# Kernel tuning notes

Measured on AMD Instinct MI355X. Metric: run time of the kernel, lower is better.

The kernel has to match this reference:

```python
import jax, jax.numpy as jnp
import numpy as np

N0, N1, N2 = 65536, 8192, 1024   # node counts per depth (pool factor 8, as in original m1*2=8)
DEG = 6                          # avg degree of k-space neighbor graphs
K = 10                           # number of Gaussian kernels in GMMConv


def _pool_graph(n_fine):
    # bidirectional edges between each group of 8 nodes and its representative (last node of group)
    mem = jnp.arange(n_fine)
    rep = (mem // 8) * 8 + 7
    return jnp.concatenate([mem, rep]), jnp.concatenate([rep, mem])


def setup_inputs() -> dict:
    key = jax.random.key(0)
    ks = list(jax.random.split(key, 40))
    E1, E2, E3 = DEG * N0, DEG * N1, DEG * N2
    d = {}
    d['n_feat'] = jax.random.normal(ks[0], (N0, 2), jnp.float32)
    d['src1'] = jax.random.randint(ks[1], (E1,), 0, N0)
    d['dst1'] = jax.random.randint(ks[2], (E1,), 0, N0)
    d['pkor1'] = 0.5 * jax.random.normal(ks[3], (E1, 2), jnp.float32)
    d['src2'] = jax.random.randint(ks[4], (E2,), 0, N1)
    d['dst2'] = jax.random.randint(ks[5], (E2,), 0, N1)
    d['pkor2'] = 0.5 * jax.random.normal(ks[6], (E2, 2), jnp.float32)
    d['src3'] = jax.random.randint(ks[7], (E3,), 0, N2)
    d['dst3'] = jax.random.randint(ks[8], (E3,), 0, N2)
    d['pkor3'] = 0.5 * jax.random.normal(ks[9], (E3, 2), jnp.float32)
    d['pm1_src'], d['pm1_dst'] = _pool_graph(N0)
    d['pm2_src'], d['pm2_dst'] = _pool_graph(N1)
    d['idx1'] = jnp.arange(N1) * 8 + 7
    d['idx2'] = jnp.arange(N2) * 8 + 7

    def lin(k, fi, fo):
        return jax.random.normal(k, (fi, K * fo), jnp.float32) / np.float32(np.sqrt(fi * K))

    d['W1'] = lin(ks[10], 2, 32)
    d['mu1'] = jax.random.normal(ks[11], (K, 2), jnp.float32)
    d['is1'] = jax.random.uniform(ks[12], (K, 2), jnp.float32, 0.5, 1.5)
    d['b1'] = 0.01 * jax.random.normal(ks[13], (32,), jnp.float32)
    d['W2'] = lin(ks[14], 32, 64)
    d['mu2'] = jax.random.normal(ks[15], (K, 2), jnp.float32)
    d['is2'] = jax.random.uniform(ks[16], (K, 2), jnp.float32, 0.5, 1.5)
    d['W3'] = lin(ks[17], 64, 128)
    d['mu3'] = jax.random.normal(ks[18], (K, 2), jnp.float32)
    d['is3'] = jax.random.uniform(ks[19], (K, 2), jnp.float32, 0.5, 1.5)
    d['W4'] = lin(ks[20], 192, 64)
    d['mu4'] = jax.random.normal(ks[21], (K, 2), jnp.float32)
    d['is4'] = jax.random.uniform(ks[22], (K, 2), jnp.float32, 0.5, 1.5)
    d['W5'] = lin(ks[23], 96, 40)
    d['mu5'] = jax.random.normal(ks[24], (K, 2), jnp.float32)
    d['is5'] = jax.random.uniform(ks[25], (K, 2), jnp.float32, 0.5, 1.5)
    d['b5'] = 0.01 * jax.random.normal(ks[26], (40,), jnp.float32)
    return d


def gmm_conv(x, W, mu, inv_sigma, src, dst, pseudo, n, bias=None):
    # DGL GMMConv, aggregator 'mean': h=fc(x) -> (N,K,F); gaussian edge weights over 2D pseudo coords
    h = (x @ W).reshape(x.shape[0], K, -1)                                   # (N,K,F)
    diff = pseudo[:, None, :] - mu[None, :, :]                               # (E,K,2)
    gw = jnp.exp(-0.5 * jnp.sum(diff * diff * (inv_sigma[None] ** 2), -1))   # (E,K)
    msg = h[src] * gw[:, :, None]                                            # (E,K,F)
    s = jax.ops.segment_sum(msg, dst, num_segments=n)
    deg = jax.ops.segment_sum(jnp.ones(dst.shape, x.dtype), dst, num_segments=n)
    out = jnp.sum(s / jnp.maximum(deg, 1.0)[:, None, None], axis=1)          # mean over edges, sum over kernels
    return out if bias is None else out + bias


def max_reduce(h, src, dst, n):
    # DGL update_all(copy_u, max): nodes with no in-edges get 0
    m = jax.ops.segment_max(h[src], dst, num_segments=n)
    deg = jax.ops.segment_sum(jnp.ones(dst.shape, h.dtype), dst, num_segments=n)
    return jnp.where(deg[:, None] > 0, m, jnp.zeros((), h.dtype))


def reference(n_feat, src1, dst1, pkor1, src2, dst2, pkor2, src3, dst3, pkor3,
              pm1_src, pm1_dst, pm2_src, pm2_dst, idx1, idx2,
              W1, mu1, is1, b1, W2, mu2, is2, W3, mu3, is3,
              W4, mu4, is4, W5, mu5, is5, b5):
    # encoder
    out0 = jax.nn.relu(gmm_conv(n_feat, W1, mu1, is1, src1, dst1, pkor1, N0, b1))      # (N0,32) skip0
    h = max_reduce(out0, pm1_src, pm1_dst, N0)[idx1]                                    # MaxPool -> (N1,32)
    out1 = jax.nn.relu(gmm_conv(h, W2, mu2, is2, src2, dst2, pkor2, N1))                # (N1,64) skip1
    h = max_reduce(out1, pm2_src, pm2_dst, N1)[idx2]                                    # MaxPool -> (N2,64)
    out2 = jax.nn.relu(gmm_conv(h, W3, mu3, is3, src3, dst3, pkor3, N2))                # (N2,128) bottleneck
    # decoder
    hu = jnp.zeros((N1, out2.shape[1]), out2.dtype).at[idx2].set(out2)
    hu = max_reduce(hu, pm2_src, pm2_dst, N1)                                           # UpSample -> (N1,128)
    out3 = jax.nn.relu(gmm_conv(jnp.concatenate([hu, out1], 1), W4, mu4, is4,
                                src2, dst2, pkor2, N1))                                 # (N1,64)
    hu = jnp.zeros((N0, out3.shape[1]), out3.dtype).at[idx1].set(out3)
    hu = max_reduce(hu, pm1_src, pm1_dst, N0)                                           # UpSample -> (N0,64)
    return jnp.tanh(gmm_conv(jnp.concatenate([hu, out0], 1), W5, mu5, is5,
                             src1, dst1, pkor1, N0, b5))                                # (N0,40)
```

## Files before the change

### kernel.cpp

```cpp
#include <hip/hip_runtime.h>


#define N0C 65536
#define N1C 8192
#define N2C 1024
#define KK 10

typedef _Float16 half2t __attribute__((ext_vector_type(2)));
typedef _Float16 half4 __attribute__((ext_vector_type(4)));
typedef _Float16 f16x8 __attribute__((ext_vector_type(8)));
typedef float f32x4 __attribute__((ext_vector_type(4)));

static inline int cdiv(long long a, long long b) { return (int)((a + b - 1) / b); }

__device__ __forceinline__ size_t fragi(int r, int kd, int KDT) {
    return ((size_t)(r >> 4) * KDT + (kd >> 5)) * 64 + ((kd >> 3) & 3) * 16 + (r & 15);
}


__global__ __launch_bounds__(256)
void k_hist3(const int* __restrict__ d1, const int* __restrict__ d2,
             const int* __restrict__ d3, int* __restrict__ g1,
             int* __restrict__ g2, int* __restrict__ g3,
             int E1, int E2, int E3) {
    int i = blockIdx.x * 256 + threadIdx.x;
    if (i < E1) atomicAdd(&g1[d1[i]], 1);
    else if (i < E1 + E2) atomicAdd(&g2[d2[i - E1]], 1);
    else if (i < E1 + E2 + E3) atomicAdd(&g3[d3[i - E1 - E2]], 1);
}

__device__ __forceinline__ void map_graph(int b, int& lb, int& gi) {
    if (b < 256) { gi = 0; lb = b; }
    else if (b < 288) { gi = 1; lb = b - 256; }
    else { gi = 2; lb = b - 288; }
}

__global__ __launch_bounds__(256)
void k_scanall(const int* __restrict__ deg1, int* __restrict__ off1, float* __restrict__ inv1,
               const int* __restrict__ deg2, int* __restrict__ off2, float* __restrict__ inv2,
               const int* __restrict__ deg3, int* __restrict__ off3, float* __restrict__ inv3,
               int E1, int E2, int E3) {
    __shared__ int s[256];
    int lb, gi; map_graph(blockIdx.x, lb, gi);
    const int* deg = gi == 0 ? deg1 : (gi == 1 ? deg2 : deg3);
    int* off = gi == 0 ? off1 : (gi == 1 ? off2 : off3);
    float* inv = gi == 0 ? inv1 : (gi == 1 ? inv2 : inv3);
    int n = gi == 0 ? N0C : (gi == 1 ? N1C : N2C);
    int E = gi == 0 ? E1 : (gi == 1 ? E2 : E3);
    int pre = 0;
    for (int i = threadIdx.x; i < lb * 256; i += 256) pre += deg[i];
    s[threadIdx.x] = pre;
    __syncthreads();
#pragma unroll
    for (int d = 128; d > 0; d >>= 1) {
        if (threadIdx.x < d) s[threadIdx.x] += s[threadIdx.x + d];
        __syncthreads();
    }
    int base = s[0];
    __syncthreads();
    int i = lb * 256 + threadIdx.x;
    int v = deg[i];
    s[threadIdx.x] = v;
    __syncthreads();
#pragma unroll
    for (int d = 1; d < 256; d <<= 1) {
        int t = (threadIdx.x >= d) ? s[threadIdx.x - d] : 0;
        __syncthreads();
        s[threadIdx.x] += t;
        __syncthreads();
    }
    off[i] = base + s[threadIdx.x] - v;
    inv[i] = 1.0f / fmaxf((float)v, 1.0f);
    if (i == n - 1) off[n] = E;
}

__global__ __launch_bounds__(256)
void k_scatter3(const int* __restrict__ s1, const int* __restrict__ d1,
                const float* __restrict__ p1, const int* __restrict__ o1,
                int* __restrict__ c1, int* __restrict__ cs1, float2* __restrict__ cp1,
                const int* __restrict__ s2, const int* __restrict__ d2,
                const float* __restrict__ p2, const int* __restrict__ o2,
                int* __restrict__ c2, int* __restrict__ cs2, float2* __restrict__ cp2,
                const int* __restrict__ s3, const int* __restrict__ d3,
                const float* __restrict__ p3, const int* __restrict__ o3,
                int* __restrict__ c3, int* __restrict__ cs3, float2* __restrict__ cp3,
                int E1, int E2, int E3) {
    int i = blockIdx.x * 256 + threadIdx.x;
    const int* src; const int* dst; const float* pk; const int* off;
    int* cur; int* csrc; float2* cpk; int e;
    if (i < E1) { src = s1; dst = d1; pk = p1; off = o1; cur = c1; csrc = cs1; cpk = cp1; e = i; }
    else if (i < E1 + E2) { src = s2; dst = d2; pk = p2; off = o2; cur = c2; csrc = cs2; cpk = cp2; e = i - E1; }
    else if (i < E1 + E2 + E3) { src = s3; dst = d3; pk = p3; off = o3; cur = c3; csrc = cs3; cpk = cp3; e = i - E1 - E2; }
    else return;
    int d = dst[e];
    int p = off[d] + atomicAdd(&cur[d], 1);
    csrc[p] = src[e];
    cpk[p] = reinterpret_cast<const float2*>(pk)[e];
}

__global__ __launch_bounds__(256)
void k_gw(const float2* __restrict__ cp1, const float2* __restrict__ cp2,
          const float2* __restrict__ cp3,
          const float* __restrict__ mu1, const float* __restrict__ is1,
          const float* __restrict__ mu5, const float* __restrict__ is5,
          const float* __restrict__ mu2, const float* __restrict__ is2,
          const float* __restrict__ mu4, const float* __restrict__ is4,
          const float* __restrict__ mu3, const float* __restrict__ is3,
          float* __restrict__ g1, float* __restrict__ g5, float* __restrict__ g2,
          float* __restrict__ g4, float* __restrict__ g3,
          int E1, int E2, int E3) {
    int i = blockIdx.x * 256 + threadIdx.x;
    const float2* cp; const float* mu; const float* isg; float* g; int e;
    if (i < E1) { cp = cp1; mu = mu1; isg = is1; g = g1; e = i; }
    else if (i < 2 * E1) { cp = cp1; mu = mu5; isg = is5; g = g5; e = i - E1; }
    else if (i < 2 * E1 + E2) { cp = cp2; mu = mu2; isg = is2; g = g2; e = i - 2 * E1; }
    else if (i < 2 * E1 + 2 * E2) { cp = cp2; mu = mu4; isg = is4; g = g4; e = i - 2 * E1 - E2; }
    else if (i < 2 * E1 + 2 * E2 + E3) { cp = cp3; mu = mu3; isg = is3; g = g3; e = i - 2 * E1 - 2 * E2; }
    else return;
    float2 pk = cp[e];
    float o[KK];
#pragma unroll
    for (int k = 0; k < KK; ++k) {
        float dx = (pk.x - mu[2 * k]) * isg[2 * k];
        float dy = (pk.y - mu[2 * k + 1]) * isg[2 * k + 1];
        o[k] = __expf(-0.5f * (dx * dx + dy * dy));
    }
    float4* gp = reinterpret_cast<float4*>(g + (size_t)e * 12);
    gp[0] = make_float4(o[0], o[1], o[2], o[3]);
    gp[1] = make_float4(o[4], o[5], o[6], o[7]);
    gp[2] = make_float4(o[8], o[9], 0.f, 0.f);
}

#define LOAD_G(gw, j, G)                                                     \
    float G[KK];                                                             \
    {                                                                        \
        const float4* gp_ = reinterpret_cast<const float4*>((gw) + (size_t)(j) * 12); \
        float4 g0_ = gp_[0], g1_ = gp_[1]; float2 g2_ = *reinterpret_cast<const float2*>(gp_ + 2); \
        G[0] = g0_.x; G[1] = g0_.y; G[2] = g0_.z; G[3] = g0_.w;              \
        G[4] = g1_.x; G[5] = g1_.y; G[6] = g1_.z; G[7] = g1_.w;              \
        G[8] = g2_.x; G[9] = g2_.y;                                          \
    }

#define LOAD_G2(gwp, j, G)                                                   \
    {                                                                        \
        const float4* gp_ = reinterpret_cast<const float4*>((gwp) + (size_t)(j) * 12); \
        float4 g0_ = gp_[0], g1_ = gp_[1];                                   \
        float2 g2_ = *reinterpret_cast<const float2*>(gp_ + 2);              \
        G[0] = g0_.x; G[1] = g0_.y; G[2] = g0_.z; G[3] = g0_.w;              \
        G[4] = g1_.x; G[5] = g1_.y; G[6] = g1_.z; G[7] = g1_.w;              \
        G[8] = g2_.x; G[9] = g2_.y;                                          \
    }

__global__ __launch_bounds__(256)
void k_prep_wt(const float* __restrict__ W1, const float* __restrict__ W2,
               const float* __restrict__ W3, const float* __restrict__ W4,
               const float* __restrict__ W5,
               _Float16* __restrict__ T2,
               _Float16* __restrict__ T3, _Float16* __restrict__ T4,
               _Float16* __restrict__ T5, int* __restrict__ degs, int degn) {
    int id = blockIdx.x * 256 + threadIdx.x;
    if (id < degn) degs[id] = 0;
    if (id < 20480) {
        int f = id / 320, kc = id % 320;
        T2[fragi(f, kc, 10) * 8 + (kc & 7)] = (_Float16)W2[(kc % 32) * 640 + (kc / 32) * 64 + f];
        return;
    }
    id -= 20480;
    if (id < 81920) {
        int f = id / 640, kc = id % 640;
        T3[fragi(f, kc, 20) * 8 + (kc & 7)] = (_Float16)W3[(kc % 64) * 1280 + (kc / 64) * 128 + f];
        return;
    }
    id -= 81920;
    if (id < 122880) {
        int f = id / 1920, kc = id % 1920;
        T4[fragi(f, kc, 60) * 8 + (kc & 7)] = (_Float16)W4[(kc % 192) * 640 + (kc / 192) * 64 + f];
        return;
    }
    id -= 122880;
    if (id < 46080) {
        int f = id / 960, kc = id % 960;
        float v = (f < 40) ? W5[(kc % 96) * 400 + (kc / 96) * 40 + f] : 0.0f;
        T5[fragi(f, kc, 30) * 8 + (kc & 7)] = (_Float16)v;
    }
}

__global__ __launch_bounds__(256, 3)
void k_l1(const float* __restrict__ x, const int* __restrict__ off,
          const int* __restrict__ csrc, const float* __restrict__ gw,
          const float* __restrict__ inv, const float* __restrict__ W1,
          const float* __restrict__ b1, _Float16* __restrict__ out0,
          _Float16* __restrict__ hp1) {
    __shared__ float Ws[640];
    __shared__ float bs[32];
    for (int i = threadIdx.x; i < 640; i += 256) Ws[i] = W1[i];
    if (threadIdx.x < 32) bs[threadIdx.x] = b1[threadIdx.x];
    __syncthreads();
    int n = blockIdx.x * 256 + threadIdx.x;
    float a0[KK], a1[KK];
#pragma unroll
    for (int k = 0; k < KK; ++k) { a0[k] = 0.f; a1[k] = 0.f; }
    int j0 = off[n], j1 = off[n + 1];
    int j = j0;
    for (; j + 1 < j1; j += 2) {
        int sa = csrc[j];
        int sb = csrc[j + 1];
        LOAD_G(gw, j, Ga)
        LOAD_G(gw, j + 1, Gb)
        float2 xa = reinterpret_cast<const float2*>(x)[sa];
        float2 xb = reinterpret_cast<const float2*>(x)[sb];
#pragma unroll
        for (int k = 0; k < KK; ++k) {
            a0[k] = fmaf(Ga[k], xa.x, a0[k]);
            a1[k] = fmaf(Ga[k], xa.y, a1[k]);
            a0[k] = fmaf(Gb[k], xb.x, a0[k]);
            a1[k] = fmaf(Gb[k], xb.y, a1[k]);
        }
    }
    if (j < j1) {
        int sa = csrc[j];
        LOAD_G(gw, j, Ga)
        float2 xa = reinterpret_cast<const float2*>(x)[sa];
#pragma unroll
        for (int k = 0; k < KK; ++k) {
            a0[k] = fmaf(Ga[k], xa.x, a0[k]);
            a1[k] = fmaf(Ga[k], xa.y, a1[k]);
        }
    }
    float iv = inv[n];
#pragma unroll
    for (int k = 0; k < KK; ++k) { a0[k] *= iv; a1[k] *= iv; }
    _Float16* orow = out0 + (size_t)n * 32;
    _Float16* prow = hp1 + (size_t)(n >> 3) * 32;
#pragma unroll
    for (int f4 = 0; f4 < 8; ++f4) {
        float v0 = bs[f4 * 4], v1 = bs[f4 * 4 + 1], v2 = bs[f4 * 4 + 2], v3 = bs[f4 * 4 + 3];
#pragma unroll
        for (int k = 0; k < KK; ++k) {
            const float* w0 = Ws + k * 32 + f4 * 4;
            const float* w1 = w0 + 320;
            v0 += a0[k] * w0[0] + a1[k] * w1[0];
            v1 += a0[k] * w0[1] + a1[k] * w1[1];
            v2 += a0[k] * w0[2] + a1[k] * w1[2];
            v3 += a0[k] * w0[3] + a1[k] * w1[3];
        }
        v0 = fmaxf(v0, 0.f); v1 = fmaxf(v1, 0.f);
        v2 = fmaxf(v2, 0.f); v3 = fmaxf(v3, 0.f);
        half4 o;
        o[0] = (_Float16)v0; o[1] = (_Float16)v1;
        o[2] = (_Float16)v2; o[3] = (_Float16)v3;
        *reinterpret_cast<half4*>(orow + f4 * 4) = o;
#pragma unroll
        for (int d = 1; d < 8; d <<= 1) {
            v0 = fmaxf(v0, __shfl_xor(v0, d));
            v1 = fmaxf(v1, __shfl_xor(v1, d));
            v2 = fmaxf(v2, __shfl_xor(v2, d));
            v3 = fmaxf(v3, __shfl_xor(v3, d));
        }
        if ((threadIdx.x & 7) == 0) {
            half4 p;
            p[0] = (_Float16)v0; p[1] = (_Float16)v1;
            p[2] = (_Float16)v2; p[3] = (_Float16)v3;
            *reinterpret_cast<half4*>(prow + f4 * 4) = p;
        }
    }
}

template <int TPN>
__global__ __launch_bounds__(256, 3)
void k_aggx(const _Float16* __restrict__ xp, const int* __restrict__ off,
            const int* __restrict__ csrc, const float* __restrict__ gw,
            const float* __restrict__ inv, _Float16* __restrict__ agg, int N) {
    constexpr int CIN = TPN * 4;
    constexpr int KDT = KK * CIN / 32;
    int tid = threadIdx.x;
    int nl = tid / TPN, tt = tid - nl * TPN;
    int node = blockIdx.x * (256 / TPN) + nl;
    if (node >= N) return;
    float a[KK][4];
#pragma unroll
    for (int k = 0; k < KK; ++k)
#pragma unroll
        for (int e = 0; e < 4; ++e) a[k][e] = 0.f;
    int j0 = off[node], j1 = off[node + 1];
    int j = j0;
    for (; j + 1 < j1; j += 2) {
        int sa = csrc[j];
        int sb = csrc[j + 1];
        LOAD_G(gw, j, Ga)
        LOAD_G(gw, j + 1, Gb)
        half4 ha = *reinterpret_cast<const half4*>(xp + (size_t)sa * CIN + 4 * tt);
        half4 hb = *reinterpret_cast<const half4*>(xp + (size_t)sb * CIN + 4 * tt);
        float a0 = ha[0], a1 = ha[1], a2 = ha[2], a3 = ha[3];
        float b0 = hb[0], b1 = hb[1], b2 = hb[2], b3 = hb[3];
#pragma unroll
        for (int k = 0; k < KK; ++k) {
            a[k][0] = fmaf(Ga[k], a0, a[k][0]);
            a[k][1] = fmaf(Ga[k], a1, a[k][1]);
            a[k][2] = fmaf(Ga[k], a2, a[k][2]);
            a[k][3] = fmaf(Ga[k], a3, a[k][3]);
            a[k][0] = fmaf(Gb[k], b0, a[k][0]);
            a[k][1] = fmaf(Gb[k], b1, a[k][1]);
            a[k][2] = fmaf(Gb[k], b2, a[k][2]);
            a[k][3] = fmaf(Gb[k], b3, a[k][3]);
        }
    }
    if (j < j1) {
        int sa = csrc[j];
        LOAD_G(gw, j, Ga)
        half4 ha = *reinterpret_cast<const half4*>(xp + (size_t)sa * CIN + 4 * tt);
        float a0 = ha[0], a1 = ha[1], a2 = ha[2], a3 = ha[3];
#pragma unroll
        for (int k = 0; k < KK; ++k) {
            a[k][0] = fmaf(Ga[k], a0, a[k][0]);
            a[k][1] = fmaf(Ga[k], a1, a[k][1]);
            a[k][2] = fmaf(Ga[k], a2, a[k][2]);
            a[k][3] = fmaf(Ga[k], a3, a[k][3]);
        }
    }
    float iv = inv[node];
#pragma unroll
    for (int k = 0; k < KK; ++k) {
        half4 o;
        o[0] = (_Float16)(a[k][0] * iv); o[1] = (_Float16)(a[k][1] * iv);
        o[2] = (_Float16)(a[k][2] * iv); o[3] = (_Float16)(a[k][3] * iv);
        int kd = k * CIN + 4 * tt;
        *reinterpret_cast<half4*>(agg + fragi(node, kd, KDT) * 8 + (kd & 7)) = o;
    }
}

template <int CA, int CB, int WPB, int NPW, int NT, int ACT, int FST, int OUTH>
__global__ __launch_bounds__(WPB * 64)
void k_aggf4(const _Float16* __restrict__ xA, const _Float16* __restrict__ xB,
             const int* __restrict__ off, const int* __restrict__ csrc,
             const float* __restrict__ gw, const float* __restrict__ inv,
             const _Float16* __restrict__ Wt, const float* __restrict__ bias,
             void* __restrict__ outv, int nodeBase) {
    constexpr int CIN = CA + CB;
    constexpr int PAIRS = CIN / 2;
    constexpr int P = (PAIRS + 63) / 64;
    constexpr int KDT = KK * CIN / 32;
    constexpr int STRIDE = KK * CIN + 8;
    __shared__ _Float16 lds[16 * STRIDE];
    const int lane = threadIdx.x & 63;
    const int wv = threadIdx.x >> 6;
    int j0u[NPW], degu[NPW], sallu[NPW];
#pragma unroll
    for (int u = 0; u < NPW; ++u) {
        const int node = __builtin_amdgcn_readfirstlane(nodeBase + blockIdx.x * 16 + wv * NPW + u);
        j0u[u] = __builtin_amdgcn_readfirstlane(off[node]);
        int j1 = __builtin_amdgcn_readfirstlane(off[node + 1]);
        degu[u] = j1 - j0u[u];
        int pl = (degu[u] > 0) ? (j0u[u] + (lane < degu[u] ? lane : degu[u] - 1)) : 0;
        sallu[u] = csrc[pl];
    }
#pragma unroll
    for (int u = 0; u < NPW; ++u) {
        const int nl = wv * NPW + u;
        const int node = __builtin_amdgcn_readfirstlane(nodeBase + blockIdx.x * 16 + nl);
        const int j0 = j0u[u];
        const int deg = degu[u];
        const int sall = sallu[u];
        float a[KK][2 * P];
#pragma unroll
        for (int k = 0; k < KK; ++k)
#pragma unroll
            for (int p = 0; p < 2 * P; ++p) a[k][p] = 0.f;
        int e = 0;
        for (; e + 1 < deg; e += 2) {
            int sa = __builtin_amdgcn_readlane(sall, e);
            int sb = __builtin_amdgcn_readlane(sall, e + 1);
            int gj = __builtin_amdgcn_readfirstlane(j0 + e);
            float Ga[KK], Gb[KK];
            LOAD_G2(gw, gj, Ga)
            LOAD_G2(gw, gj + 1, Gb)
            float xa0[P], xa1[P], xb0[P], xb1[P];
#pragma unroll
            for (int p = 0; p < P; ++p) {
                int c0 = 2 * (lane + 64 * p);
                xa0[p] = 0.f; xa1[p] = 0.f; xb0[p] = 0.f; xb1[p] = 0.f;
                if (c0 < CIN) {
                    bool useA = c0 < CA;
                    const _Float16* qa = useA ? (xA + (size_t)(sa >> 3) * CA + c0)
                                              : (xB + (size_t)sa * CB + (c0 - CA));
                    const _Float16* qb = useA ? (xA + (size_t)(sb >> 3) * CA + c0)
                                              : (xB + (size_t)sb * CB + (c0 - CA));
                    half2t ha = *reinterpret_cast<const half2t*>(qa);
                    half2t hb = *reinterpret_cast<const half2t*>(qb);
                    xa0[p] = ha[0]; xa1[p] = ha[1];
                    xb0[p] = hb[0]; xb1[p] = hb[1];
                }
            }
#pragma unroll
            for (int k = 0; k < KK; ++k)
#pragma unroll
                for (int p = 0; p < P; ++p) {
                    a[k][2 * p] = fmaf(Ga[k], xa0[p], a[k][2 * p]);
                    a[k][2 * p + 1] = fmaf(Ga[k], xa1[p], a[k][2 * p + 1]);
                    a[k][2 * p] = fmaf(Gb[k], xb0[p], a[k][2 * p]);
                    a[k][2 * p + 1] = fmaf(Gb[k], xb1[p], a[k][2 * p + 1]);
                }
        }
        if (e < deg) {
            int sa = __builtin_amdgcn_readlane(sall, e);
            int gj = __builtin_amdgcn_readfirstlane(j0 + e);
            float Ga[KK];
            LOAD_G2(gw, gj, Ga)
            float xa0[P], xa1[P];
#pragma unroll
            for (int p = 0; p < P; ++p) {
                int c0 = 2 * (lane + 64 * p);
                xa0[p] = 0.f; xa1[p] = 0.f;
                if (c0 < CIN) {
                    const _Float16* qa = (c0 < CA) ? (xA + (size_t)(sa >> 3) * CA + c0)
                                                   : (xB + (size_t)sa * CB + (c0 - CA));
                    half2t ha = *reinterpret_cast<const half2t*>(qa);
                    xa0[p] = ha[0]; xa1[p] = ha[1];
                }
            }
#pragma unroll
            for (int k = 0; k < KK; ++k)
#pragma unroll
                for (int p = 0; p < P; ++p) {
                    a[k][2 * p] = fmaf(Ga[k], xa0[p], a[k][2 * p]);
                    a[k][2 * p + 1] = fmaf(Ga[k], xa1[p], a[k][2 * p + 1]);
                }
        }
        float iv = inv[node];
#pragma unroll
        for (int k = 0; k < KK; ++k)
#pragma unroll
            for (int p = 0; p < P; ++p) {
                int c0 = 2 * (lane + 64 * p);
                if (c0 < CIN) {
                    half2t o;
                    o[0] = (_Float16)(a[k][2 * p] * iv);
                    o[1] = (_Float16)(a[k][2 * p + 1] * iv);
                    *reinterpret_cast<half2t*>(&lds[nl * STRIDE + k * CIN + c0]) = o;
                }
            }
    }
    constexpr int PF = (KDT < 8) ? KDT : 8;
    const int lm = lane & 15;
    const int q = lane >> 4;
    const f16x8* bp = (const f16x8*)Wt + (size_t)wv * KDT * 64 + lane;
    f16x8 bfr[PF];
    if (wv < NT) {
#pragma unroll
        for (int i = 0; i < PF; ++i) bfr[i] = bp[(size_t)i * 64];
    }
    __syncthreads();
    if (wv < NT) {
        f32x4 acc = (f32x4){0.f, 0.f, 0.f, 0.f};
        f16x8 af = *reinterpret_cast<const f16x8*>(&lds[lm * STRIDE + q * 8]);
#pragma unroll
        for (int i = 0; i < KDT; ++i) {
            f16x8 afn;
            if (i + 1 < KDT)
                afn = *reinterpret_cast<const f16x8*>(&lds[lm * STRIDE + (i + 1) * 32 + q * 8]);
            f16x8 b = bfr[i % PF];
            if (i + PF < KDT) bfr[i % PF] = bp[(size_t)(i + PF) * 64];
            acc = __builtin_amdgcn_mfma_f32_16x16x32_f16(af, b, acc, 0, 0, 0);
            af = afn;
        }
        int f = wv * 16 + lm;
        if (f < FST) {
            float b = bias ? bias[f] : 0.0f;
#pragma unroll
            for (int r = 0; r < 4; ++r) {
                size_t node = (size_t)nodeBase + (size_t)blockIdx.x * 16 + q * 4 + r;
                float v = acc[r] + b;
                v = (ACT == 1) ? tanhf(v) : fmaxf(v, 0.0f);
                if (OUTH) ((_Float16*)outv)[node * FST + f] = (_Float16)v;
                else ((float*)outv)[node * FST + f] = v;
            }
        }
    }
}

template <int WB, int NT, int ITERS, int ACT, int FST, int OUTH, int POOL>
__global__ __launch_bounds__(WB * 64)
void k_gemm2(const _Float16* __restrict__ A, const _Float16* __restrict__ B,
             const float* __restrict__ bias, void* __restrict__ outv,
             _Float16* __restrict__ poolout, int M) {
    constexpr int KDT = ITERS;
    const int lane = threadIdx.x & 63;
    const int wv = threadIdx.x >> 6;
    const int lm = lane & 15;
    const int q = lane >> 4;
    const size_t m0 = (size_t)blockIdx.y * (WB * 16) + wv * 16;
    const size_t mblk = m0 >> 4;
    f32x4 acc[NT];
#pragma unroll
    for (int t = 0; t < NT; ++t) acc[t] = (f32x4){0.f, 0.f, 0.f, 0.f};
    const f16x8* ap = (const f16x8*)A + mblk * KDT * 64 + lane;
    const f16x8* bp = (const f16x8*)B + lane;
    f16x8 af = ap[0];
    f16x8 bf[NT];
#pragma unroll
    for (int t = 0; t < NT; ++t) bf[t] = bp[(size_t)t * KDT * 64];
#pragma unroll
    for (int i = 0; i < ITERS; ++i) {
        f16x8 afn; f16x8 bfn[NT];
        if (i + 1 < ITERS) {
            afn = ap[(size_t)(i + 1) * 64];
#pragma unroll
            for (int t = 0; t < NT; ++t)
                bfn[t] = bp[((size_t)t * KDT + i + 1) * 64];
        }
#pragma unroll
        for (int t = 0; t < NT; ++t)
            acc[t] = __builtin_amdgcn_mfma_f32_16x16x32_f16(af, bf[t], acc[t], 0, 0, 0);
        af = afn;
#pragma unroll
        for (int t = 0; t < NT; ++t) bf[t] = bfn[t];
    }
#pragma unroll
    for (int t = 0; t < NT; ++t) {
        int f = t * 16 + lm;
        if (f < FST) {
            float b = bias ? bias[f] : 0.0f;
            float vr[4];
#pragma unroll
            for (int r = 0; r < 4; ++r) {
                float v = acc[t][r] + b;
                vr[r] = (ACT == 1) ? tanhf(v) : fmaxf(v, 0.0f);
            }
#pragma unroll
            for (int r = 0; r < 4; ++r) {
                if (OUTH) ((_Float16*)outv)[(m0 + q * 4 + r) * (size_t)FST + f] = (_Float16)vr[r];
                else ((float*)outv)[(m0 + q * 4 + r) * (size_t)FST + f] = vr[r];
            }
            if (POOL) {
                float m = fmaxf(fmaxf(vr[0], vr[1]), fmaxf(vr[2], vr[3]));
                m = fmaxf(m, __shfl_xor(m, 16));
                if ((q & 1) == 0)
                    poolout[(size_t)((m0 >> 3) + (q >> 1)) * FST + f] = (_Float16)m;
            }
        }
    }
}

extern "C" void kernel_launch(void* const* d_in, const int* in_sizes, int n_in,
                              void* d_out, int out_size, void* d_ws, size_t ws_size,
                              hipStream_t stream) {
    const float* n_feat = (const float*)d_in[0];
    const int* src1 = (const int*)d_in[1];
    const int* dst1 = (const int*)d_in[2];
    const float* pkor1 = (const float*)d_in[3];
    const int* src2 = (const int*)d_in[4];
    const int* dst2 = (const int*)d_in[5];
    const float* pkor2 = (const float*)d_in[6];
    const int* src3 = (const int*)d_in[7];
    const int* dst3 = (const int*)d_in[8];
    const float* pkor3 = (const float*)d_in[9];
    const float* W1 = (const float*)d_in[16];
    const float* mu1 = (const float*)d_in[17];
    const float* is1 = (const float*)d_in[18];
    const float* b1 = (const float*)d_in[19];
    const float* W2 = (const float*)d_in[20];
    const float* mu2 = (const float*)d_in[21];
    const float* is2 = (const float*)d_in[22];
    const float* W3 = (const float*)d_in[23];
    const float* mu3 = (const float*)d_in[24];
    const float* is3 = (const float*)d_in[25];
    const float* W4 = (const float*)d_in[26];
    const float* mu4 = (const float*)d_in[27];
    const float* is4 = (const float*)d_in[28];
    const float* W5 = (const float*)d_in[29];
    const float* mu5 = (const float*)d_in[30];
    const float* is5 = (const float*)d_in[31];
    const float* b5 = (const float*)d_in[32];

    const int E1 = in_sizes[1], E2 = in_sizes[4], E3 = in_sizes[7];
    const int NT_ = N0C + N1C + N2C;

    char* w = (char*)d_ws;
    auto alloc = [&](size_t bytes) {
        void* p = (void*)w;
        w += (bytes + 255) & ~(size_t)255;
        return p;
    };
    int* degs = (int*)alloc((size_t)NT_ * 2 * 4);
    int* deg1 = degs, *deg2 = degs + N0C, *deg3 = degs + N0C + N1C;
    int* cur1 = degs + NT_, *cur2 = cur1 + N0C, *cur3 = cur2 + N1C;
    int* off1 = (int*)alloc(((size_t)N0C + 1) * 4);
    int* off2 = (int*)alloc(((size_t)N1C + 1) * 4);
    int* off3 = (int*)alloc(((size_t)N2C + 1) * 4);
    int* csrc1 = (int*)alloc((size_t)E1 * 4);
    float2* cpk1 = (float2*)alloc((size_t)E1 * 8);
    int* csrc2 = (int*)alloc((size_t)E2 * 4);
    float2* cpk2 = (float2*)alloc((size_t)E2 * 8);
    int* csrc3 = (int*)alloc((size_t)E3 * 4);
    float2* cpk3 = (float2*)alloc((size_t)E3 * 8);
    float* inv1 = (float*)alloc((size_t)N0C * 4);
    float* inv2 = (float*)alloc((size_t)N1C * 4);
    float* inv3 = (float*)alloc((size_t)N2C * 4);
    float* g1 = (float*)alloc(((size_t)2 * E1 + 2 * E2 + E3) * 12 * 4);
    float* g5 = g1 + (size_t)E1 * 12;
    float* g2 = g5 + (size_t)E1 * 12;
    float* g4 = g2 + (size_t)E2 * 12;
    float* g3 = g4 + (size_t)E2 * 12;
    _Float16* out0 = (_Float16*)alloc((size_t)N0C * 32 * 2);
    _Float16* out1 = (_Float16*)alloc((size_t)N1C * 64 * 2);
    _Float16* out2 = (_Float16*)alloc((size_t)N2C * 128 * 2);
    _Float16* out3 = (_Float16*)alloc((size_t)N1C * 64 * 2);
    _Float16* hp1 = (_Float16*)alloc((size_t)N1C * 32 * 2);
    _Float16* hp2 = (_Float16*)alloc((size_t)N2C * 64 * 2);
    _Float16* agg2 = (_Float16*)alloc((size_t)N1C * 320 * 2);
    _Float16* agg3 = (_Float16*)alloc((size_t)N2C * 640 * 2);
    _Float16* Wt2 = (_Float16*)alloc((size_t)64 * 320 * 2);
    _Float16* Wt3 = (_Float16*)alloc((size_t)128 * 640 * 2);
    _Float16* Wt4 = (_Float16*)alloc((size_t)64 * 1920 * 2);
    _Float16* Wt5 = (_Float16*)alloc((size_t)48 * 960 * 2);

    const int ET = E1 + E2 + E3;
    const int GT = 2 * E1 + 2 * E2 + E3;

    k_prep_wt<<<cdiv(271360, 256), 256, 0, stream>>>(W1, W2, W3, W4, W5,
                                                     Wt2, Wt3, Wt4, Wt5,
                                                     degs, NT_ * 2);
    k_hist3<<<cdiv(ET, 256), 256, 0, stream>>>(dst1, dst2, dst3, deg1, deg2, deg3, E1, E2, E3);
    k_scanall<<<292, 256, 0, stream>>>(deg1, off1, inv1, deg2, off2, inv2,
                                       deg3, off3, inv3, E1, E2, E3);
    k_scatter3<<<cdiv(ET, 256), 256, 0, stream>>>(
        src1, dst1, pkor1, off1, cur1, csrc1, cpk1,
        src2, dst2, pkor2, off2, cur2, csrc2, cpk2,
        src3, dst3, pkor3, off3, cur3, csrc3, cpk3, E1, E2, E3);
    k_gw<<<cdiv(GT, 256), 256, 0, stream>>>(
        cpk1, cpk2, cpk3, mu1, is1, mu5, is5, mu2, is2, mu4, is4, mu3, is3,
        g1, g5, g2, g4, g3, E1, E2, E3);

    k_l1<<<N0C / 256, 256, 0, stream>>>(n_feat, off1, csrc1, g1, inv1, W1, b1, out0, hp1);

    k_aggx<8><<<cdiv(N1C, 32), 256, 0, stream>>>(hp1, off2, csrc2, g2, inv2, agg2, N1C);
    k_gemm2<2, 4, 10, 0, 64, 1, 1><<<dim3(1, N1C / 32), 128, 0, stream>>>(agg2, Wt2, nullptr, out1, hp2, N1C);

    k_aggx<16><<<cdiv(N2C, 16), 256, 0, stream>>>(hp2, off3, csrc3, g3, inv3, agg3, N2C);
    k_gemm2<1, 8, 20, 0, 128, 1, 0><<<dim3(1, N2C / 16), 64, 0, stream>>>(agg3, Wt3, nullptr, out2, nullptr, N2C);

    k_aggf4<128, 64, 16, 1, 4, 0, 64, 1><<<N1C / 16, 1024, 0, stream>>>(
        out2, out1, off2, csrc2, g4, inv2, Wt4, nullptr, out3, 0);

    k_aggf4<64, 32, 8, 2, 3, 1, 40, 0><<<N0C / 16, 512, 0, stream>>>(
        out3, out0, off1, csrc1, g5, inv1, Wt5, b5, d_out, 0);
}
```

Baseline: 334.1 us.

## Split edge loops across threads and software-pipeline gather loads in aggregation kernels

k_l1 now uses two threads per node, each walking alternate edges, and combines their partial sums with a shuffle. The two threads split the output features, and the max-pool shuffle is remapped to match. k_aggx gains an ES parameter so several thread groups split one node's edges and reduce with xor-shuffles, with more blocks launched to match. k_aggf4 gains a PIPE mode, enabled for the last layer, that prefetches the next edge pair's Gaussian weights and features before doing the current FMAs. The goal is more parallelism and better hiding of latency on the irregular gathers, at the cost of extra shuffles, more registers and idle lanes when nodes have few edges.

Result: slower. 382.8 us (+14.6%).

```diff
diff --git a/kernel.cpp b/kernel.cpp
--- a/kernel.cpp
+++ b/kernel.cpp
@@ -131,16 +131,6 @@
     gp[2] = make_float4(o[8], o[9], 0.f, 0.f);
 }
 
-#define LOAD_G(gw, j, G)                                                     \
-    float G[KK];                                                             \
-    {                                                                        \
-        const float4* gp_ = reinterpret_cast<const float4*>((gw) + (size_t)(j) * 12); \
-        float4 g0_ = gp_[0], g1_ = gp_[1]; float2 g2_ = *reinterpret_cast<const float2*>(gp_ + 2); \
-        G[0] = g0_.x; G[1] = g0_.y; G[2] = g0_.z; G[3] = g0_.w;              \
-        G[4] = g1_.x; G[5] = g1_.y; G[6] = g1_.z; G[7] = g1_.w;              \
-        G[8] = g2_.x; G[9] = g2_.y;                                          \
-    }
-
 #define LOAD_G2(gwp, j, G)                                                   \
     {                                                                        \
         const float4* gp_ = reinterpret_cast<const float4*>((gwp) + (size_t)(j) * 12); \
@@ -196,44 +186,53 @@
     for (int i = threadIdx.x; i < 640; i += 256) Ws[i] = W1[i];
     if (threadIdx.x < 32) bs[threadIdx.x] = b1[threadIdx.x];
     __syncthreads();
-    int n = blockIdx.x * 256 + threadIdx.x;
+    int tid2 = blockIdx.x * 256 + threadIdx.x;
+    int n = tid2 >> 1;
+    int h = tid2 & 1;
     float a0[KK], a1[KK];
 #pragma unroll
     for (int k = 0; k < KK; ++k) { a0[k] = 0.f; a1[k] = 0.f; }
     int j0 = off[n], j1 = off[n + 1];
-    int j = j0;
-    for (; j + 1 < j1; j += 2) {
-        int sa = csrc[j];
-        int sb = csrc[j + 1];
-        LOAD_G(gw, j, Ga)
-        LOAD_G(gw, j + 1, Gb)
-        float2 xa = reinterpret_cast<const float2*>(x)[sa];
-        float2 xb = reinterpret_cast<const float2*>(x)[sb];
+    int j = j0 + h;
+    bool have = j < j1;
+    float Gc[KK]; float2 xc;
+    if (have) {
+        int s = csrc[j];
+        LOAD_G2(gw, j, Gc)
+        xc = reinterpret_cast<const float2*>(x)[s];
+    }
+    while (have) {
+        int jn = j + 2;
+        bool hn = jn < j1;
+        float Gn[KK]; float2 xn;
+        if (hn) {
+            int s = csrc[jn];
+            LOAD_G2(gw, jn, Gn)
+            xn = reinterpret_cast<const float2*>(x)[s];
+        }
 #pragma unroll
         for (int k = 0; k < KK; ++k) {
-            a0[k] = fmaf(Ga[k], xa.x, a0[k]);
-            a1[k] = fmaf(Ga[k], xa.y, a1[k]);
-            a0[k] = fmaf(Gb[k], xb.x, a0[k]);
-            a1[k] = fmaf(Gb[k], xb.y, a1[k]);
-        }
-    }
-    if (j < j1) {
-        int sa = csrc[j];
-        LOAD_G(gw, j, Ga)
-        float2 xa = reinterpret_cast<const float2*>(x)[sa];
-#pragma unroll
-        for (int k = 0; k < KK; ++k) {
-            a0[k] = fmaf(Ga[k], xa.x, a0[k]);
-            a1[k] = fmaf(Ga[k], xa.y, a1[k]);
+            a0[k] = fmaf(Gc[k], xc.x, a0[k]);
+            a1[k] = fmaf(Gc[k], xc.y, a1[k]);
+        }
+        j = jn; have = hn;
+        if (hn) {
+#pragma unroll
+            for (int k = 0; k < KK; ++k) Gc[k] = Gn[k];
+            xc = xn;
         }
     }
     float iv = inv[n];
 #pragma unroll
-    for (int k = 0; k < KK; ++k) { a0[k] *= iv; a1[k] *= iv; }
+    for (int k = 0; k < KK; ++k) {
+        a0[k] = (a0[k] + __shfl_xor(a0[k], 1)) * iv;
+        a1[k] = (a1[k] + __shfl_xor(a1[k], 1)) * iv;
+    }
     _Float16* orow = out0 + (size_t)n * 32;
-    _Float16* prow = hp1 + (size_t)(n >> 3) * 32;
-#pragma unroll
-    for (int f4 = 0; f4 < 8; ++f4) {
+    _Float16* prow = hp1 + (size_t)(tid2 >> 4) * 32;
+#pragma unroll
+    for (int t = 0; t < 4; ++t) {
+        int f4 = h * 4 + t;
         float v0 = bs[f4 * 4], v1 = bs[f4 * 4 + 1], v2 = bs[f4 * 4 + 2], v3 = bs[f4 * 4 + 3];
 #pragma unroll
         for (int k = 0; k < KK; ++k) {
@@ -251,13 +250,13 @@
         o[2] = (_Float16)v2; o[3] = (_Float16)v3;
         *reinterpret_cast<half4*>(orow + f4 * 4) = o;
 #pragma unroll
-        for (int d = 1; d < 8; d <<= 1) {
+        for (int d = 2; d < 16; d <<= 1) {
             v0 = fmaxf(v0, __shfl_xor(v0, d));
             v1 = fmaxf(v1, __shfl_xor(v1, d));
             v2 = fmaxf(v2, __shfl_xor(v2, d));
             v3 = fmaxf(v3, __shfl_xor(v3, d));
         }
-        if ((threadIdx.x & 7) == 0) {
+        if ((threadIdx.x & 15) == h) {
             half4 p;
             p[0] = (_Float16)v0; p[1] = (_Float16)v1;
             p[2] = (_Float16)v2; p[3] = (_Float16)v3;
@@ -266,16 +265,18 @@
     }
 }
 
-template <int TPN>
+template <int TPN, int ES>
 __global__ __launch_bounds__(256, 3)
 void k_aggx(const _Float16* __restrict__ xp, const int* __restrict__ off,
             const int* __restrict__ csrc, const float* __restrict__ gw,
             const float* __restrict__ inv, _Float16* __restrict__ agg, int N) {
     constexpr int CIN = TPN * 4;
     constexpr int KDT = KK * CIN / 32;
-    int tid = threadIdx.x;
-    int nl = tid / TPN, tt = tid - nl * TPN;
-    int node = blockIdx.x * (256 / TPN) + nl;
+    constexpr int TG = TPN * ES;
+    int gtid = blockIdx.x * 256 + threadIdx.x;
+    int node = gtid / TG;
+    int rem = threadIdx.x % TG;
+    int tt = rem % TPN, es = rem / TPN;
     if (node >= N) return;
     float a[KK][4];
 #pragma unroll
@@ -283,53 +284,62 @@
 #pragma unroll
         for (int e = 0; e < 4; ++e) a[k][e] = 0.f;
     int j0 = off[node], j1 = off[node + 1];
-    int j = j0;
-    for (; j + 1 < j1; j += 2) {
-        int sa = csrc[j];
-        int sb = csrc[j + 1];
-        LOAD_G(gw, j, Ga)
-        LOAD_G(gw, j + 1, Gb)
-        half4 ha = *reinterpret_cast<const half4*>(xp + (size_t)sa * CIN + 4 * tt);
-        half4 hb = *reinterpret_cast<const half4*>(xp + (size_t)sb * CIN + 4 * tt);
-        float a0 = ha[0], a1 = ha[1], a2 = ha[2], a3 = ha[3];
-        float b0 = hb[0], b1 = hb[1], b2 = hb[2], b3 = hb[3];
+    const _Float16* xb = xp + 4 * tt;
+    int j = j0 + es;
+    bool have = j < j1;
+    float Gc[KK]; half4 hc;
+    if (have) {
+        int s = csrc[j];
+        LOAD_G2(gw, j, Gc)
+        hc = *reinterpret_cast<const half4*>(xb + (size_t)s * CIN);
+    }
+    while (have) {
+        int jn = j + ES;
+        bool hn = jn < j1;
+        float Gn[KK]; half4 hx;
+        if (hn) {
+            int s = csrc[jn];
+            LOAD_G2(gw, jn, Gn)
+            hx = *reinterpret_cast<const half4*>(xb + (size_t)s * CIN);
+        }
+        float f0 = hc[0], f1 = hc[1], f2 = hc[2], f3 = hc[3];
 #pragma unroll
         for (int k = 0; k < KK; ++k) {
-            a[k][0] = fmaf(Ga[k], a0, a[k][0]);
-            a[k][1] = fmaf(Ga[k], a1, a[k][1]);
-            a[k][2] = fmaf(Ga[k], a2, a[k][2]);
-            a[k][3] = fmaf(Ga[k], a3, a[k][3]);
-            a[k][0] = fmaf(Gb[k], b0, a[k][0]);
-            a[k][1] = fmaf(Gb[k], b1, a[k][1]);
-            a[k][2] = fmaf(Gb[k], b2, a[k][2]);
-            a[k][3] = fmaf(Gb[k], b3, a[k][3]);
-        }
-    }
-    if (j < j1) {
-        int sa = csrc[j];
-        LOAD_G(gw, j, Ga)
-        half4 ha = *reinterpret_cast<const half4*>(xp + (size_t)sa * CIN + 4 * tt);
-        float a0 = ha[0], a1 = ha[1], a2 = ha[2], a3 = ha[3];
+            a[k][0] = fmaf(Gc[k], f0, a[k][0]);
+            a[k][1] = fmaf(Gc[k], f1, a[k][1]);
+            a[k][2] = fmaf(Gc[k], f2, a[k][2]);
+            a[k][3] = fmaf(Gc[k], f3, a[k][3]);
+        }
+        j = jn; have = hn;
+        if (hn) {
+#pragma unroll
+            for (int k = 0; k < KK; ++k) Gc[k] = Gn[k];
+            hc = hx;
+        }
+    }
+#pragma unroll
+    for (int d = TPN; d < TG; d <<= 1)
 #pragma unroll
         for (int k = 0; k < KK; ++k) {
-            a[k][0] = fmaf(Ga[k], a0, a[k][0]);
-            a[k][1] = fmaf(Ga[k], a1, a[k][1]);
-            a[k][2] = fmaf(Ga[k], a2, a[k][2]);
-            a[k][3] = fmaf(Ga[k], a3, a[k][3]);
-        }
-    }
-    float iv = inv[node];
-#pragma unroll
-    for (int k = 0; k < KK; ++k) {
-        half4 o;
-        o[0] = (_Float16)(a[k][0] * iv); o[1] = (_Float16)(a[k][1] * iv);
-        o[2] = (_Float16)(a[k][2] * iv); o[3] = (_Float16)(a[k][3] * iv);
-        int kd = k * CIN + 4 * tt;
-        *reinterpret_cast<half4*>(agg + fragi(node, kd, KDT) * 8 + (kd & 7)) = o;
-    }
-}
-
-template <int CA, int CB, int WPB, int NPW, int NT, int ACT, int FST, int OUTH>
+            a[k][0] += __shfl_xor(a[k][0], d);
+            a[k][1] += __shfl_xor(a[k][1], d);
+            a[k][2] += __shfl_xor(a[k][2], d);
+            a[k][3] += __shfl_xor(a[k][3], d);
+        }
+    if (es == 0) {
+        float iv = inv[node];
+#pragma unroll
+        for (int k = 0; k < KK; ++k) {
+            half4 o;
+            o[0] = (_Float16)(a[k][0] * iv); o[1] = (_Float16)(a[k][1] * iv);
+            o[2] = (_Float16)(a[k][2] * iv); o[3] = (_Float16)(a[k][3] * iv);
+            int kd = k * CIN + 4 * tt;
+            *reinterpret_cast<half4*>(agg + fragi(node, kd, KDT) * 8 + (kd & 7)) = o;
+        }
+    }
+}
+
+template <int CA, int CB, int WPB, int NPW, int NT, int ACT, int FST, int OUTH, int PIPE>
 __global__ __launch_bounds__(WPB * 64)
 void k_aggf4(const _Float16* __restrict__ xA, const _Float16* __restrict__ xB,
              const int* __restrict__ off, const int* __restrict__ csrc,
@@ -354,6 +364,51 @@
         int pl = (degu[u] > 0) ? (j0u[u] + (lane < degu[u] ? lane : degu[u] - 1)) : 0;
         sallu[u] = csrc[pl];
     }
+
+#define AGG_LOADP(I, GA, GB, XA0, XA1, XB0, XB1)                              \
+    {                                                                         \
+        int e0_ = 2 * (I);                                                    \
+        bool odd_ = (e0_ + 1) >= deg;                                         \
+        int e1c_ = odd_ ? deg - 1 : e0_ + 1;                                  \
+        int sa_ = __builtin_amdgcn_readlane(sall, e0_);                       \
+        int sb_ = __builtin_amdgcn_readlane(sall, e1c_);                      \
+        int gja_ = __builtin_amdgcn_readfirstlane(j0 + e0_);                  \
+        int gjb_ = __builtin_amdgcn_readfirstlane(j0 + e1c_);                 \
+        LOAD_G2(gw, gja_, GA)                                                 \
+        LOAD_G2(gw, gjb_, GB)                                                 \
+        if (odd_) {                                                           \
+            _Pragma("unroll")                                                 \
+            for (int k_ = 0; k_ < KK; ++k_) GB[k_] = 0.f;                     \
+        }                                                                     \
+        _Pragma("unroll")                                                     \
+        for (int p_ = 0; p_ < P; ++p_) {                                      \
+            int c0_ = 2 * (lane + 64 * p_);                                   \
+            XA0[p_] = 0.f; XA1[p_] = 0.f; XB0[p_] = 0.f; XB1[p_] = 0.f;       \
+            if (c0_ < CIN) {                                                  \
+                bool useA_ = c0_ < CA;                                        \
+                const _Float16* qa_ = useA_ ? (xA + (size_t)(sa_ >> 3) * CA + c0_) \
+                                            : (xB + (size_t)sa_ * CB + (c0_ - CA)); \
+                const _Float16* qb_ = useA_ ? (xA + (size_t)(sb_ >> 3) * CA + c0_) \
+                                            : (xB + (size_t)sb_ * CB + (c0_ - CA)); \
+                half2t ha_ = *reinterpret_cast<const half2t*>(qa_);           \
+                half2t hb_ = *reinterpret_cast<const half2t*>(qb_);           \
+                XA0[p_] = ha_[0]; XA1[p_] = ha_[1];                           \
+                XB0[p_] = hb_[0]; XB1[p_] = hb_[1];                           \
+            }                                                                 \
+        }                                                                     \
+    }
+
+#define AGG_FMA(GA, GB, XA0, XA1, XB0, XB1)                                   \
+    _Pragma("unroll")                                                         \
+    for (int k_ = 0; k_ < KK; ++k_)                                           \
+        _Pragma("unroll")                                                     \
+        for (int p_ = 0; p_ < P; ++p_) {                                      \
+            a[k_][2 * p_] = fmaf(GA[k_], XA0[p_], a[k_][2 * p_]);             \
+            a[k_][2 * p_ + 1] = fmaf(GA[k_], XA1[p_], a[k_][2 * p_ + 1]);     \
+            a[k_][2 * p_] = fmaf(GB[k_], XB0[p_], a[k_][2 * p_]);             \
+            a[k_][2 * p_ + 1] = fmaf(GB[k_], XB1[p_], a[k_][2 * p_ + 1]);     \
+        }
+
 #pragma unroll
     for (int u = 0; u < NPW; ++u) {
         const int nl = wv * NPW + u;
@@ -366,65 +421,78 @@
         for (int k = 0; k < KK; ++k)
 #pragma unroll
             for (int p = 0; p < 2 * P; ++p) a[k][p] = 0.f;
-        int e = 0;
-        for (; e + 1 < deg; e += 2) {
-            int sa = __builtin_amdgcn_readlane(sall, e);
-            int sb = __builtin_amdgcn_readlane(sall, e + 1);
-            int gj = __builtin_amdgcn_readfirstlane(j0 + e);
-            float Ga[KK], Gb[KK];
-            LOAD_G2(gw, gj, Ga)
-            LOAD_G2(gw, gj + 1, Gb)
-            float xa0[P], xa1[P], xb0[P], xb1[P];
-#pragma unroll
-            for (int p = 0; p < P; ++p) {
-                int c0 = 2 * (lane + 64 * p);
-                xa0[p] = 0.f; xa1[p] = 0.f; xb0[p] = 0.f; xb1[p] = 0.f;
-                if (c0 < CIN) {
-                    bool useA = c0 < CA;
-                    const _Float16* qa = useA ? (xA + (size_t)(sa >> 3) * CA + c0)
-                                              : (xB + (size_t)sa * CB + (c0 - CA));
-                    const _Float16* qb = useA ? (xA + (size_t)(sb >> 3) * CA + c0)
-                                              : (xB + (size_t)sb * CB + (c0 - CA));
-                    half2t ha = *reinterpret_cast<const half2t*>(qa);
-                    half2t hb = *reinterpret_cast<const half2t*>(qb);
-                    xa0[p] = ha[0]; xa1[p] = ha[1];
-                    xb0[p] = hb[0]; xb1[p] = hb[1];
+        if (PIPE) {
+            int np = (deg + 1) >> 1;
+            float Ga[KK], Gb[KK], xa0[P], xa1[P], xb0[P], xb1[P];
+            if (np > 0) AGG_LOADP(0, Ga, Gb, xa0, xa1, xb0, xb1)
+            for (int i = 0; i < np; ++i) {
+                float Gan[KK], Gbn[KK], xa0n[P], xa1n[P], xb0n[P], xb1n[P];
+                bool hn = (i + 1 < np);
+                if (hn) AGG_LOADP(i + 1, Gan, Gbn, xa0n, xa1n, xb0n, xb1n)
+                AGG_FMA(Ga, Gb, xa0, xa1, xb0, xb1)
+                if (hn) {
+#pragma unroll
+                    for (int k2 = 0; k2 < KK; ++k2) { Ga[k2] = Gan[k2]; Gb[k2] = Gbn[k2]; }
+#pragma unroll
+                    for (int p2 = 0; p2 < P; ++p2) {
+                        xa0[p2] = xa0n[p2]; xa1[p2] = xa1n[p2];
+                        xb0[p2] = xb0n[p2]; xb1[p2] = xb1n[p2];
+                    }
                 }
             }
-#pragma unroll
-            for (int k = 0; k < KK; ++k)
+        } else {
+            int e = 0;
+            for (; e + 1 < deg; e += 2) {
+                int sa = __builtin_amdgcn_readlane(sall, e);
+                int sb = __builtin_amdgcn_readlane(sall, e + 1);
+                int gj = __builtin_amdgcn_readfirstlane(j0 + e);
+                float Ga[KK], Gb[KK];
+                LOAD_G2(gw, gj, Ga)
+                LOAD_G2(gw, gj + 1, Gb)
+                float xa0[P], xa1[P], xb0[P], xb1[P];
 #pragma unroll
                 for (int p = 0; p < P; ++p) {
-                    a[k][2 * p] = fmaf(Ga[k], xa0[p], a[k][2 * p]);
-                    a[k][2 * p + 1] = fmaf(Ga[k], xa1[p], a[k][2 * p + 1]);
-                    a[k][2 * p] = fmaf(Gb[k], xb0[p], a[k][2 * p]);
-                    a[k][2 * p + 1] = fmaf(Gb[k], xb1[p], a[k][2 * p + 1]);
+                    int c0 = 2 * (lane + 64 * p);
+                    xa0[p] = 0.f; xa1[p] = 0.f; xb0[p] = 0.f; xb1[p] = 0.f;
+                    if (c0 < CIN) {
+                        bool useA = c0 < CA;
+                        const _Float16* qa = useA ? (xA + (size_t)(sa >> 3) * CA + c0)
+                                                  : (xB + (size_t)sa * CB + (c0 - CA));
+                        const _Float16* qb = useA ? (xA + (size_t)(sb >> 3) * CA + c0)
+                                                  : (xB + (size_t)sb * CB + (c0 - CA));
+                        half2t ha = *reinterpret_cast<const half2t*>(qa);
+                        half2t hb = *reinterpret_cast<const half2t*>(qb);
+                        xa0[p] = ha[0]; xa1[p] = ha[1];
+                        xb0[p] = hb[0]; xb1[p] = hb[1];
+                    }
                 }
-        }
-        if (e < deg) {
-            int sa = __builtin_amdgcn_readlane(sall, e);
-            int gj = __builtin_amdgcn_readfirstlane(j0 + e);
-            float Ga[KK];
-            LOAD_G2(gw, gj, Ga)
-            float xa0[P], xa1[P];
-#pragma unroll
-            for (int p = 0; p < P; ++p) {
-                int c0 = 2 * (lane + 64 * p);
-                xa0[p] = 0.f; xa1[p] = 0.f;
-                if (c0 < CIN) {
-                    const _Float16* qa = (c0 < CA) ? (xA + (size_t)(sa >> 3) * CA + c0)
-                                                   : (xB + (size_t)sa * CB + (c0 - CA));
-                    half2t ha = *reinterpret_cast<const half2t*>(qa);
-                    xa0[p] = ha[0]; xa1[p] = ha[1];
+                AGG_FMA(Ga, Gb, xa0, xa1, xb0, xb1)
+            }
+            if (e < deg) {
+                int sa = __builtin_amdgcn_readlane(sall, e);
+                int gj = __builtin_amdgcn_readfirstlane(j0 + e);
+                float Ga[KK];
+                LOAD_G2(gw, gj, Ga)
+                float xa0[P], xa1[P];
+#pragma unroll
+                for (int p = 0; p < P; ++p) {
+                    int c0 = 2 * (lane + 64 * p);
+                    xa0[p] = 0.f; xa1[p] = 0.f;
+                    if (c0 < CIN) {
+                        const _Float16* qa = (c0 < CA) ? (xA + (size_t)(sa >> 3) * CA + c0)
+                                                       : (xB + (size_t)sa * CB + (c0 - CA));
+                        half2t ha = *reinterpret_cast<const half2t*>(qa);
+                        xa0[p] = ha[0]; xa1[p] = ha[1];
+                    }
                 }
+#pragma unroll
+                for (int k = 0; k < KK; ++k)
+#pragma unroll
+                    for (int p = 0; p < P; ++p) {
+                        a[k][2 * p] = fmaf(Ga[k], xa0[p], a[k][2 * p]);
+                        a[k][2 * p + 1] = fmaf(Ga[k], xa1[p], a[k][2 * p + 1]);
+                    }
             }
-#pragma unroll
-            for (int k = 0; k < KK; ++k)
-#pragma unroll
-                for (int p = 0; p < P; ++p) {
-                    a[k][2 * p] = fmaf(Ga[k], xa0[p], a[k][2 * p]);
-                    a[k][2 * p + 1] = fmaf(Ga[k], xa1[p], a[k][2 * p + 1]);
-                }
         }
         float iv = inv[node];
 #pragma unroll
@@ -440,6 +508,8 @@
                 }
             }
     }
+#undef AGG_LOADP
+#undef AGG_FMA
     constexpr int PF = (KDT < 8) ? KDT : 8;
     const int lm = lane & 15;
     const int q = lane >> 4;
@@ -631,17 +701,17 @@
         cpk1, cpk2, cpk3, mu1, is1, mu5, is5, mu2, is2, mu4, is4, mu3, is3,
         g1, g5, g2, g4, g3, E1, E2, E3);
 
-    k_l1<<<N0C / 256, 256, 0, stream>>>(n_feat, off1, csrc1, g1, inv1, W1, b1, out0, hp1);
-
-    k_aggx<8><<<cdiv(N1C, 32), 256, 0, stream>>>(hp1, off2, csrc2, g2, inv2, agg2, N1C);
+    k_l1<<<N0C * 2 / 256, 256, 0, stream>>>(n_feat, off1, csrc1, g1, inv1, W1, b1, out0, hp1);
+
+    k_aggx<8, 2><<<cdiv((size_t)N1C * 16, 256), 256, 0, stream>>>(hp1, off2, csrc2, g2, inv2, agg2, N1C);
     k_gemm2<2, 4, 10, 0, 64, 1, 1><<<dim3(1, N1C / 32), 128, 0, stream>>>(agg2, Wt2, nullptr, out1, hp2, N1C);
 
-    k_aggx<16><<<cdiv(N2C, 16), 256, 0, stream>>>(hp2, off3, csrc3, g3, inv3, agg3, N2C);
+    k_aggx<16, 4><<<cdiv((size_t)N2C * 64, 256), 256, 0, stream>>>(hp2, off3, csrc3, g3, inv3, agg3, N2C);
     k_gemm2<1, 8, 20, 0, 128, 1, 0><<<dim3(1, N2C / 16), 64, 0, stream>>>(agg3, Wt3, nullptr, out2, nullptr, N2C);
 
-    k_aggf4<128, 64, 16, 1, 4, 0, 64, 1><<<N1C / 16, 1024, 0, stream>>>(
+    k_aggf4<128, 64, 16, 1, 4, 0, 64, 1, 0><<<N1C / 16, 1024, 0, stream>>>(
         out2, out1, off2, csrc2, g4, inv2, Wt4, nullptr, out3, 0);
 
-    k_aggf4<64, 32, 8, 2, 3, 1, 40, 0><<<N0C / 16, 512, 0, stream>>>(
+    k_aggf4<64, 32, 8, 2, 3, 1, 40, 0, 1><<<N0C / 16, 512, 0, stream>>>(
         out3, out0, off1, csrc1, g5, inv1, Wt5, b5, d_out, 0);
 }
```
